# Kernel tuning notes

Hardware: AMD Instinct MI355X
Metric: run time of the kernel (lower is better)

## Reference

```python
import jax, jax.numpy as jnp
import numpy as np

N_NODES = 50000
N_EDGES = 600000
D_FEAT = 128


def setup_inputs() -> dict:
    key = jax.random.key(0)
    k_h, k_src, k_dst, k_dt, k_norm = jax.random.split(key, 5)
    h = jax.random.normal(k_h, (N_NODES, D_FEAT), dtype=jnp.float32)
    src = jax.random.randint(k_src, (N_EDGES,), 0, N_NODES, dtype=jnp.int32)
    dst = jax.random.randint(k_dst, (N_EDGES,), 0, N_NODES, dtype=jnp.int32)
    # dt: non-negative time deltas (scaled up a bit so the decay matters)
    dt = jax.random.uniform(k_dt, (N_EDGES,), dtype=jnp.float32) * 10.0
    # norm: symmetric-normalization-like positive edge weights
    norm = jax.random.uniform(k_norm, (N_EDGES,), dtype=jnp.float32)
    decay_lam = jnp.full((1,), 0.1, dtype=jnp.float32)  # nn.Parameter(0.1)
    return {"h": h, "src": src, "dst": dst, "dt": dt, "norm": norm, "decay_lam": decay_lam}


def reference(h, src, dst, dt, norm, decay_lam):
    # lam = relu(decay_lam) + 1e-4  (scalar)
    lam = jax.nn.relu(decay_lam[0]) + 1e-4
    # per-edge temporal weight: norm * exp(-lam * dt)   [E]
    w = norm * jnp.exp(-lam * dt)
    # u_mul_e: gather source features, scale by edge weight  [E, D]
    m = h[src] * w[:, None]
    # sum-reduce messages at destination nodes  [N, D]
    h_new = jax.ops.segment_sum(m, dst, num_segments=h.shape[0])
    return h_new
```

## Files before the change

### kernel.cpp

```cpp
#include <hip/hip_runtime.h>
#include <hip/hip_bf16.h>

#define D_FEAT 128
#define PAD 32
#define OVF_CAP 4096

typedef float f2v __attribute__((ext_vector_type(2)));

__device__ __forceinline__ unsigned bf16_rne(float f) {
    unsigned u = __float_as_uint(f);
    return (u + 0x7fffu + ((u >> 16) & 1u)) >> 16;
}

__global__ void conv_bucket_kernel(const float* __restrict__ h,
                                   const int* __restrict__ src, const int* __restrict__ dst,
                                   const float* __restrict__ dt, const float* __restrict__ norm,
                                   const float* __restrict__ decay_lam,
                                   unsigned* __restrict__ hb,
                                   int* __restrict__ cursor, unsigned* __restrict__ pairs,
                                   int* __restrict__ ovf_cnt, int* __restrict__ ovf_d,
                                   int* __restrict__ ovf_s, float* __restrict__ ovf_w,
                                   int E, int HN4, int convBlocks) {
    int bid = blockIdx.x;
    if (bid < convBlocks) {
        int i = bid * 256 + threadIdx.x;
        if (i < HN4) {
            float4 v = ((const float4*)h)[i];
            unsigned lo = bf16_rne(v.x) | (bf16_rne(v.y) << 16);
            unsigned hi = bf16_rne(v.z) | (bf16_rne(v.w) << 16);
            ((uint2*)hb)[i] = make_uint2(lo, hi);
        }
    } else {
        int e = (bid - convBlocks) * 256 + threadIdx.x;
        if (e >= E) return;
        float lam = fmaxf(decay_lam[0], 0.0f) + 1e-4f;
        float w = norm[e] * expf(-lam * dt[e]);
        int d = dst[e];
        int s = src[e];
        int pos = atomicAdd(&cursor[d], 1);
        if (pos < PAD) {
            pairs[(size_t)d * PAD + pos] = ((unsigned)s << 16) | bf16_rne(w);
        } else {
            int o = atomicAdd(ovf_cnt, 1);
            if (o < OVF_CAP) { ovf_d[o] = d; ovf_s[o] = s; ovf_w[o] = w; }
        }
    }
}

__global__ void __launch_bounds__(256)
gather_pad_kernel(const unsigned* __restrict__ hb, const int* __restrict__ cursor,
                  const unsigned* __restrict__ pairs,
                  const int* __restrict__ ovf_cnt, const int* __restrict__ ovf_d,
                  const int* __restrict__ ovf_s, const float* __restrict__ ovf_w,
                  float* __restrict__ out, int N) {
    int node = blockIdx.x * 4 + (threadIdx.x >> 6);
    if (node >= N) return;
    int lane = threadIdx.x & 63;
    int deg = cursor[node];
    int m = min(deg, PAD);

    unsigned pu = 0;
    if (lane < m) pu = pairs[(size_t)node * PAD + lane];

    int mr = (m + 7) & ~7;

    float accx = 0.0f, accy = 0.0f;
    for (int j = 0; j < mr; j += 8) {
        unsigned u0 = __shfl(pu, j + 0, 64);
        unsigned u1 = __shfl(pu, j + 1, 64);
        unsigned u2 = __shfl(pu, j + 2, 64);
        unsigned u3 = __shfl(pu, j + 3, 64);
        unsigned u4 = __shfl(pu, j + 4, 64);
        unsigned u5 = __shfl(pu, j + 5, 64);
        unsigned u6 = __shfl(pu, j + 6, 64);
        unsigned u7 = __shfl(pu, j + 7, 64);
        unsigned v0 = hb[(size_t)(u0 >> 16) * 64 + lane];
        unsigned v1 = hb[(size_t)(u1 >> 16) * 64 + lane];
        unsigned v2 = hb[(size_t)(u2 >> 16) * 64 + lane];
        unsigned v3 = hb[(size_t)(u3 >> 16) * 64 + lane];
        unsigned v4 = hb[(size_t)(u4 >> 16) * 64 + lane];
        unsigned v5 = hb[(size_t)(u5 >> 16) * 64 + lane];
        unsigned v6 = hb[(size_t)(u6 >> 16) * 64 + lane];
        unsigned v7 = hb[(size_t)(u7 >> 16) * 64 + lane];
        #define ACC(u, v)                                             \
        {   float wf = __uint_as_float((u) << 16);                    \
            float vx = __uint_as_float((v) << 16);                    \
            float vy = __uint_as_float((v) & 0xffff0000u);            \
            accx += vx * wf; accy += vy * wf; }
        ACC(u0, v0) ACC(u1, v1) ACC(u2, v2) ACC(u3, v3)
        ACC(u4, v4) ACC(u5, v5) ACC(u6, v6) ACC(u7, v7)
        #undef ACC
    }

    if (deg > PAD) {
        int oc = min(*ovf_cnt, OVF_CAP);
        for (int o = 0; o < oc; ++o) {
            if (ovf_d[o] == node) {
                float we = ovf_w[o];
                unsigned v = hb[(size_t)ovf_s[o] * 64 + lane];
                accx += __uint_as_float(v << 16) * we;
                accy += __uint_as_float(v & 0xffff0000u) * we;
            }
        }
    }
    f2v r;
    r.x = accx; r.y = accy;
    __builtin_nontemporal_store(r, (f2v*)(out + (size_t)node * D_FEAT) + lane);
}


__global__ void degree_kernel(const int* __restrict__ dst, int* __restrict__ deg, int E) {
    int e = blockIdx.x * blockDim.x + threadIdx.x;
    if (e >= E) return;
    atomicAdd(&deg[dst[e]], 1);
}

__global__ void scan_blocks(const int* __restrict__ deg, int* __restrict__ offs,
                            int* __restrict__ blockSums, int N) {
    __shared__ int tmp[256];
    int tid = threadIdx.x;
    int gid = blockIdx.x * 256 + tid;
    int v = (gid < N) ? deg[gid] : 0;
    tmp[tid] = v;
    __syncthreads();
    for (int off = 1; off < 256; off <<= 1) {
        int t = (tid >= off) ? tmp[tid - off] : 0;
        __syncthreads();
        tmp[tid] += t;
        __syncthreads();
    }
    if (gid < N) offs[gid] = tmp[tid] - v;
    if (tid == 255) blockSums[blockIdx.x] = tmp[255];
}

__global__ void scan_sums(int* __restrict__ blockSums, int* __restrict__ blockOffs, int nb) {
    __shared__ int tmp[256];
    int tid = threadIdx.x;
    int v = (tid < nb) ? blockSums[tid] : 0;
    tmp[tid] = v;
    __syncthreads();
    for (int off = 1; off < 256; off <<= 1) {
        int t = (tid >= off) ? tmp[tid - off] : 0;
        __syncthreads();
        tmp[tid] += t;
        __syncthreads();
    }
    if (tid < nb) blockOffs[tid] = tmp[tid] - v;
}

__global__ void scan_fixup(int* __restrict__ offs, const int* __restrict__ blockOffs,
                           int* __restrict__ cursor, int N) {
    int gid = blockIdx.x * 256 + threadIdx.x;
    if (gid >= N) return;
    int o = offs[gid] + blockOffs[blockIdx.x];
    offs[gid] = o;
    cursor[gid] = o;
}

__global__ void bucket_kernel(const int* __restrict__ src, const int* __restrict__ dst,
                              const float* __restrict__ dt, const float* __restrict__ norm,
                              const float* __restrict__ decay_lam,
                              int* __restrict__ cursor, float2* __restrict__ pairs, int E) {
    int e = blockIdx.x * blockDim.x + threadIdx.x;
    if (e >= E) return;
    float lam = fmaxf(decay_lam[0], 0.0f) + 1e-4f;
    float w = norm[e] * expf(-lam * dt[e]);
    int d = dst[e];
    int pos = atomicAdd(&cursor[d], 1);
    float2 p;
    p.x = __int_as_float(src[e]);
    p.y = w;
    pairs[pos] = p;
}

__global__ void __launch_bounds__(256)
gather_kernel(const float* __restrict__ h,
              const int* __restrict__ offs, const int* __restrict__ deg,
              const float2* __restrict__ pairs, float* __restrict__ out, int N) {
    int node = blockIdx.x * 4 + (threadIdx.x >> 6);
    if (node >= N) return;
    int lane = threadIdx.x & 63;
    int start = offs[node];
    int end = start + deg[node];
    float accx = 0.0f, accy = 0.0f;
    for (int j = start; j < end; ++j) {
        float2 p = pairs[j];
        int s = __float_as_int(p.x);
        float we = p.y;
        float2 v = ((const float2*)(h + (size_t)s * D_FEAT))[lane];
        accx += v.x * we;
        accy += v.y * we;
    }
    float2 r; r.x = accx; r.y = accy;
    ((float2*)(out + (size_t)node * D_FEAT))[lane] = r;
}

extern "C" void kernel_launch(void* const* d_in, const int* in_sizes, int n_in,
                              void* d_out, int out_size, void* d_ws, size_t ws_size,
                              hipStream_t stream) {
    const float* h         = (const float*)d_in[0];
    const int*   src       = (const int*)d_in[1];
    const int*   dst       = (const int*)d_in[2];
    const float* dt        = (const float*)d_in[3];
    const float* norm      = (const float*)d_in[4];
    const float* decay_lam = (const float*)d_in[5];
    float* out = (float*)d_out;

    const int E  = in_sizes[1];
    const int HN = in_sizes[0];
    const int N  = out_size / D_FEAT;

    size_t pad_need = (size_t)N * 4
                    + 64
                    + (size_t)OVF_CAP * 12
                    + (size_t)N * PAD * 4
                    + (size_t)HN * 2;

    if (ws_size >= pad_need && N <= 65536 && (HN & 3) == 0) {
        char* ws = (char*)d_ws;
        int*      cursor  = (int*)ws;       ws += (size_t)N * 4;
        int*      ovf_cnt = (int*)ws;       ws += 64;
        int*      ovf_d   = (int*)ws;       ws += (size_t)OVF_CAP * 4;
        int*      ovf_s   = (int*)ws;       ws += (size_t)OVF_CAP * 4;
        float*    ovf_w   = (float*)ws;     ws += (size_t)OVF_CAP * 4;
        unsigned* pairs   = (unsigned*)ws;  ws += (size_t)N * PAD * 4;
        unsigned* hb      = (unsigned*)ws;

        hipMemsetAsync(cursor, 0, (size_t)N * 4 + 64, stream);

        const int HN4 = HN / 4;
        const int convBlocks = (HN4 + 255) / 256;
        const int bucketBlocks = (E + 255) / 256;
        conv_bucket_kernel<<<convBlocks + bucketBlocks, 256, 0, stream>>>(
            h, src, dst, dt, norm, decay_lam, hb, cursor, pairs,
            ovf_cnt, ovf_d, ovf_s, ovf_w, E, HN4, convBlocks);

        gather_pad_kernel<<<(N + 3) / 4, 256, 0, stream>>>(
            hb, cursor, pairs, ovf_cnt, ovf_d, ovf_s, ovf_w, out, N);
    } else {
        const int nb = (N + 255) / 256;
        char* ws = (char*)d_ws;
        int*    deg       = (int*)ws;     ws += (size_t)N * 4;
        int*    offs      = (int*)ws;     ws += (size_t)N * 4;
        int*    cursor    = (int*)ws;     ws += (size_t)N * 4;
        int*    blockSums = (int*)ws;     ws += 256 * 4;
        int*    blockOffs = (int*)ws;     ws += 256 * 4;
        float2* pairs     = (float2*)ws;

        hipMemsetAsync(deg, 0, (size_t)N * 4, stream);
        degree_kernel<<<(E + 255) / 256, 256, 0, stream>>>(dst, deg, E);
        scan_blocks<<<nb, 256, 0, stream>>>(deg, offs, blockSums, N);
        scan_sums<<<1, 256, 0, stream>>>(blockSums, blockOffs, nb);
        scan_fixup<<<nb, 256, 0, stream>>>(offs, blockOffs, cursor, N);
        bucket_kernel<<<(E + 255) / 256, 256, 0, stream>>>(
            src, dst, dt, norm, decay_lam, cursor, pairs, E);
        gather_kernel<<<(N + 3) / 4, 256, 0, stream>>>(h, offs, deg, pairs, out, N);
    }
}
```

Before: 156.1 us.

## Replace per-node atomic padded buckets with two-level binned counting sort into CSR

Replaces the per-edge global atomic append into fixed 32-slot per-node buckets with a two-pass sort. Each block first stages 4096 edges in shared memory, bins them by groups of 128 destination nodes, and writes them out with a few global atomics per bin. A per-bin kernel then counting-sorts each bin into a compact CSR with offsets and degrees. The goal is to cut contended global atomics and the scattered padded writes. The cost is an extra kernel launch, extra passes over 8-byte binned entries, and a separate launch for the bf16 conversion of h.

Measured after the change: 130.5 us. 16.4% less time.

```diff
diff --git a/kernel.cpp b/kernel.cpp
--- a/kernel.cpp
+++ b/kernel.cpp
@@ -2,7 +2,11 @@
 #include <hip/hip_bf16.h>
 
 #define D_FEAT 128
-#define PAD 32
+#define BIN_SHIFT 7
+#define NODES_PER_BIN 128
+#define BCAP 4096
+#define EPB 4096
+#define T1 512
 #define OVF_CAP 4096
 
 typedef float f2v __attribute__((ext_vector_type(2)));
@@ -12,56 +16,164 @@
     return (u + 0x7fffu + ((u >> 16) & 1u)) >> 16;
 }
 
-__global__ void conv_bucket_kernel(const float* __restrict__ h,
-                                   const int* __restrict__ src, const int* __restrict__ dst,
-                                   const float* __restrict__ dt, const float* __restrict__ norm,
-                                   const float* __restrict__ decay_lam,
-                                   unsigned* __restrict__ hb,
-                                   int* __restrict__ cursor, unsigned* __restrict__ pairs,
-                                   int* __restrict__ ovf_cnt, int* __restrict__ ovf_d,
-                                   int* __restrict__ ovf_s, float* __restrict__ ovf_w,
-                                   int E, int HN4, int convBlocks) {
-    int bid = blockIdx.x;
-    if (bid < convBlocks) {
-        int i = bid * 256 + threadIdx.x;
-        if (i < HN4) {
-            float4 v = ((const float4*)h)[i];
-            unsigned lo = bf16_rne(v.x) | (bf16_rne(v.y) << 16);
-            unsigned hi = bf16_rne(v.z) | (bf16_rne(v.w) << 16);
-            ((uint2*)hb)[i] = make_uint2(lo, hi);
-        }
-    } else {
-        int e = (bid - convBlocks) * 256 + threadIdx.x;
-        if (e >= E) return;
-        float lam = fmaxf(decay_lam[0], 0.0f) + 1e-4f;
-        float w = norm[e] * expf(-lam * dt[e]);
-        int d = dst[e];
-        int s = src[e];
-        int pos = atomicAdd(&cursor[d], 1);
-        if (pos < PAD) {
-            pairs[(size_t)d * PAD + pos] = ((unsigned)s << 16) | bf16_rne(w);
-        } else {
-            int o = atomicAdd(ovf_cnt, 1);
-            if (o < OVF_CAP) { ovf_d[o] = d; ovf_s[o] = s; ovf_w[o] = w; }
+__global__ void conv_kernel(const float* __restrict__ h, unsigned* __restrict__ hb, int HN4) {
+    int i = blockIdx.x * 256 + threadIdx.x;
+    if (i >= HN4) return;
+    float4 v = ((const float4*)h)[i];
+    ((uint2*)hb)[i] = make_uint2(bf16_rne(v.x) | (bf16_rne(v.y) << 16),
+                                 bf16_rne(v.z) | (bf16_rne(v.w) << 16));
+}
+
+__global__ void __launch_bounds__(T1)
+bin_kernel(const int* __restrict__ src, const int* __restrict__ dst,
+           const float* __restrict__ dt, const float* __restrict__ norm,
+           const float* __restrict__ decay_lam,
+           int* __restrict__ bin_cursor, unsigned long long* __restrict__ binned,
+           int* __restrict__ ovf_cnt, int* __restrict__ ovf_d,
+           int* __restrict__ ovf_s, float* __restrict__ ovf_w,
+           int E, int NB) {
+    __shared__ unsigned hist[T1];
+    __shared__ unsigned tmp[T1];
+    __shared__ unsigned cur[T1];
+    __shared__ unsigned gbase[T1];
+    __shared__ unsigned long long stage[EPB];
+    __shared__ unsigned gaddr[EPB];
+
+    int t = threadIdx.x;
+    int e0 = blockIdx.x * EPB;
+    int cnt_blk = min(EPB, E - e0);
+
+    hist[t] = 0; cur[t] = 0; gbase[t] = 0;
+    __syncthreads();
+
+    float lam = fmaxf(decay_lam[0], 0.0f) + 1e-4f;
+
+    unsigned long long ent[EPB / T1];
+    int bn[EPB / T1];
+    #pragma unroll
+    for (int k = 0; k < EPB / T1; ++k) {
+        int e = e0 + k * T1 + t;
+        bn[k] = -1;
+        if (e < E) {
+            int s = src[e], d = dst[e];
+            float w = norm[e] * expf(-lam * dt[e]);
+            int b = d >> BIN_SHIFT;
+            int l = d & (NODES_PER_BIN - 1);
+            ent[k] = ((unsigned long long)l << 32) | (((unsigned)s << 16) | bf16_rne(w));
+            bn[k] = b;
+            atomicAdd(&hist[b], 1u);
+        }
+    }
+    __syncthreads();
+    tmp[t] = hist[t];
+    __syncthreads();
+    for (int off = 1; off < T1; off <<= 1) {
+        unsigned v = (t >= off) ? tmp[t - off] : 0;
+        __syncthreads();
+        tmp[t] += v;
+        __syncthreads();
+    }
+    unsigned base_t = tmp[t] - hist[t];
+    if (t < NB && hist[t] > 0)
+        gbase[t] = (unsigned)atomicAdd(&bin_cursor[t], (int)hist[t]);
+    __syncthreads();
+    tmp[t] = base_t;
+    __syncthreads();
+
+    #pragma unroll
+    for (int k = 0; k < EPB / T1; ++k) {
+        if (bn[k] >= 0) {
+            int b = bn[k];
+            unsigned loc = atomicAdd(&cur[b], 1u);
+            unsigned p = tmp[b] + loc;
+            unsigned gp = gbase[b] + loc;
+            stage[p] = ent[k];
+            if (gp < BCAP) {
+                gaddr[p] = (unsigned)b * BCAP + gp;
+            } else {
+                gaddr[p] = 0xFFFFFFFFu;
+                int o = atomicAdd(ovf_cnt, 1);
+                if (o < OVF_CAP) {
+                    int l = (int)(ent[k] >> 32);
+                    ovf_d[o] = (b << BIN_SHIFT) | l;
+                    ovf_s[o] = (int)((ent[k] >> 16) & 0xFFFFu);
+                    ovf_w[o] = __uint_as_float(((unsigned)ent[k] & 0xFFFFu) << 16);
+                }
+            }
+        }
+    }
+    __syncthreads();
+    #pragma unroll
+    for (int k = 0; k < EPB / T1; ++k) {
+        int idx = k * T1 + t;
+        if (idx < cnt_blk) {
+            unsigned g = gaddr[idx];
+            if (g != 0xFFFFFFFFu) binned[g] = stage[idx];
         }
     }
 }
 
 __global__ void __launch_bounds__(256)
-gather_pad_kernel(const unsigned* __restrict__ hb, const int* __restrict__ cursor,
-                  const unsigned* __restrict__ pairs,
-                  const int* __restrict__ ovf_cnt, const int* __restrict__ ovf_d,
-                  const int* __restrict__ ovf_s, const float* __restrict__ ovf_w,
-                  float* __restrict__ out, int N) {
+sort_kernel(const unsigned long long* __restrict__ binned, const int* __restrict__ bin_cursor,
+            unsigned* __restrict__ csr, int* __restrict__ offs, int* __restrict__ deg,
+            int N, int NB) {
+    __shared__ unsigned hist[NODES_PER_BIN];
+    __shared__ unsigned tmp[NODES_PER_BIN];
+    __shared__ unsigned cur[NODES_PER_BIN];
+    int b = blockIdx.x;
+    int t = threadIdx.x;
+    int cnt = min(bin_cursor[b], BCAP);
+    if (t < NODES_PER_BIN) { hist[t] = 0; cur[t] = 0; }
+    __syncthreads();
+    size_t base_in = (size_t)b * BCAP;
+    for (int i = t; i < cnt; i += 256) {
+        int l = (int)(binned[base_in + i] >> 32);
+        atomicAdd(&hist[l], 1u);
+    }
+    __syncthreads();
+    if (t < NODES_PER_BIN) tmp[t] = hist[t];
+    __syncthreads();
+    for (int off = 1; off < NODES_PER_BIN; off <<= 1) {
+        unsigned v = 0;
+        if (t < NODES_PER_BIN && t >= off) v = tmp[t - off];
+        __syncthreads();
+        if (t < NODES_PER_BIN) tmp[t] += v;
+        __syncthreads();
+    }
+    if (t < NODES_PER_BIN) {
+        int node = (b << BIN_SHIFT) + t;
+        unsigned loff = tmp[t] - hist[t];
+        if (node < N) {
+            offs[node] = b * BCAP + (int)loff;
+            deg[node]  = (int)hist[t];
+        }
+        tmp[t] = loff;
+    }
+    __syncthreads();
+    for (int i = t; i < cnt; i += 256) {
+        unsigned long long e = binned[base_in + i];
+        int l = (int)(e >> 32);
+        unsigned p = tmp[l] + atomicAdd(&cur[l], 1u);
+        csr[base_in + p] = (unsigned)e;
+    }
+}
+
+__global__ void __launch_bounds__(256)
+gather_kernel2(const unsigned* __restrict__ hb, const int* __restrict__ offs,
+               const int* __restrict__ deg, const unsigned* __restrict__ csr,
+               const int* __restrict__ bin_cursor,
+               const int* __restrict__ ovf_cnt, const int* __restrict__ ovf_d,
+               const int* __restrict__ ovf_s, const float* __restrict__ ovf_w,
+               float* __restrict__ out, int N) {
     int node = blockIdx.x * 4 + (threadIdx.x >> 6);
     if (node >= N) return;
     int lane = threadIdx.x & 63;
-    int deg = cursor[node];
-    int m = min(deg, PAD);
+    int dg = deg[node];
+    int base = offs[node];
+    int m = min(dg, 64);
 
     unsigned pu = 0;
-    if (lane < m) pu = pairs[(size_t)node * PAD + lane];
-
+    if (lane < m) pu = csr[base + lane];
     int mr = (m + 7) & ~7;
 
     float accx = 0.0f, accy = 0.0f;
@@ -91,8 +203,14 @@
         ACC(u4, v4) ACC(u5, v5) ACC(u6, v6) ACC(u7, v7)
         #undef ACC
     }
-
-    if (deg > PAD) {
+    for (int j = 64; j < dg; ++j) {
+        unsigned u = csr[base + j];
+        float wf = __uint_as_float(u << 16);
+        unsigned v = hb[(size_t)(u >> 16) * 64 + lane];
+        accx += __uint_as_float(v << 16) * wf;
+        accy += __uint_as_float(v & 0xffff0000u) * wf;
+    }
+    if (bin_cursor[node >> BIN_SHIFT] > BCAP) {
         int oc = min(*ovf_cnt, OVF_CAP);
         for (int o = 0; o < oc; ++o) {
             if (ovf_d[o] == node) {
@@ -209,51 +327,57 @@
     const int E  = in_sizes[1];
     const int HN = in_sizes[0];
     const int N  = out_size / D_FEAT;
-
-    size_t pad_need = (size_t)N * 4
-                    + 64
-                    + (size_t)OVF_CAP * 12
-                    + (size_t)N * PAD * 4
-                    + (size_t)HN * 2;
-
-    if (ws_size >= pad_need && N <= 65536 && (HN & 3) == 0) {
+    const int NB = (N + NODES_PER_BIN - 1) >> BIN_SHIFT;
+
+    auto align64 = [](size_t x) { return (x + 63) & ~(size_t)63; };
+    size_t sz_binc = align64((size_t)NB * 4);
+    size_t sz_ovfc = 64;
+    size_t sz_ovf  = align64((size_t)OVF_CAP * 4);
+    size_t sz_offs = align64((size_t)N * 4);
+    size_t sz_binn = align64((size_t)NB * BCAP * 8);
+    size_t sz_csr  = align64((size_t)NB * BCAP * 4);
+    size_t sz_hb   = align64((size_t)HN * 2);
+    size_t need = sz_binc + sz_ovfc + 3 * sz_ovf + 2 * sz_offs + sz_binn + sz_csr + sz_hb;
+
+    if (ws_size >= need && N <= 65536 && (HN & 3) == 0) {
         char* ws = (char*)d_ws;
-        int*      cursor  = (int*)ws;       ws += (size_t)N * 4;
-        int*      ovf_cnt = (int*)ws;       ws += 64;
-        int*      ovf_d   = (int*)ws;       ws += (size_t)OVF_CAP * 4;
-        int*      ovf_s   = (int*)ws;       ws += (size_t)OVF_CAP * 4;
-        float*    ovf_w   = (float*)ws;     ws += (size_t)OVF_CAP * 4;
-        unsigned* pairs   = (unsigned*)ws;  ws += (size_t)N * PAD * 4;
-        unsigned* hb      = (unsigned*)ws;
-
-        hipMemsetAsync(cursor, 0, (size_t)N * 4 + 64, stream);
-
-        const int HN4 = HN / 4;
-        const int convBlocks = (HN4 + 255) / 256;
-        const int bucketBlocks = (E + 255) / 256;
-        conv_bucket_kernel<<<convBlocks + bucketBlocks, 256, 0, stream>>>(
-            h, src, dst, dt, norm, decay_lam, hb, cursor, pairs,
-            ovf_cnt, ovf_d, ovf_s, ovf_w, E, HN4, convBlocks);
-
-        gather_pad_kernel<<<(N + 3) / 4, 256, 0, stream>>>(
-            hb, cursor, pairs, ovf_cnt, ovf_d, ovf_s, ovf_w, out, N);
+        int* bin_cursor = (int*)ws;                 ws += sz_binc;
+        int* ovf_cnt    = (int*)ws;                 ws += sz_ovfc;
+        int* ovf_d      = (int*)ws;                 ws += sz_ovf;
+        int* ovf_s      = (int*)ws;                 ws += sz_ovf;
+        float* ovf_w    = (float*)ws;               ws += sz_ovf;
+        int* offs       = (int*)ws;                 ws += sz_offs;
+        int* deg        = (int*)ws;                 ws += sz_offs;
+        unsigned long long* binned = (unsigned long long*)ws;  ws += sz_binn;
+        unsigned* csr   = (unsigned*)ws;            ws += sz_csr;
+        unsigned* hb    = (unsigned*)ws;
+
+        hipMemsetAsync(bin_cursor, 0, sz_binc + sz_ovfc, stream);
+
+        conv_kernel<<<(HN / 4 + 255) / 256, 256, 0, stream>>>(h, hb, HN / 4);
+        bin_kernel<<<(E + EPB - 1) / EPB, T1, 0, stream>>>(
+            src, dst, dt, norm, decay_lam, bin_cursor, binned,
+            ovf_cnt, ovf_d, ovf_s, ovf_w, E, NB);
+        sort_kernel<<<NB, 256, 0, stream>>>(binned, bin_cursor, csr, offs, deg, N, NB);
+        gather_kernel2<<<(N + 3) / 4, 256, 0, stream>>>(
+            hb, offs, deg, csr, bin_cursor, ovf_cnt, ovf_d, ovf_s, ovf_w, out, N);
     } else {
         const int nb = (N + 255) / 256;
         char* ws = (char*)d_ws;
-        int*    deg       = (int*)ws;     ws += (size_t)N * 4;
-        int*    offs      = (int*)ws;     ws += (size_t)N * 4;
+        int*    dega      = (int*)ws;     ws += (size_t)N * 4;
+        int*    offsa     = (int*)ws;     ws += (size_t)N * 4;
         int*    cursor    = (int*)ws;     ws += (size_t)N * 4;
         int*    blockSums = (int*)ws;     ws += 256 * 4;
         int*    blockOffs = (int*)ws;     ws += 256 * 4;
         float2* pairs     = (float2*)ws;
 
-        hipMemsetAsync(deg, 0, (size_t)N * 4, stream);
-        degree_kernel<<<(E + 255) / 256, 256, 0, stream>>>(dst, deg, E);
-        scan_blocks<<<nb, 256, 0, stream>>>(deg, offs, blockSums, N);
+        hipMemsetAsync(dega, 0, (size_t)N * 4, stream);
+        degree_kernel<<<(E + 255) / 256, 256, 0, stream>>>(dst, dega, E);
+        scan_blocks<<<nb, 256, 0, stream>>>(dega, offsa, blockSums, N);
         scan_sums<<<1, 256, 0, stream>>>(blockSums, blockOffs, nb);
-        scan_fixup<<<nb, 256, 0, stream>>>(offs, blockOffs, cursor, N);
+        scan_fixup<<<nb, 256, 0, stream>>>(offsa, blockOffs, cursor, N);
         bucket_kernel<<<(E + 255) / 256, 256, 0, stream>>>(
             src, dst, dt, norm, decay_lam, cursor, pairs, E);
-        gather_kernel<<<(N + 3) / 4, 256, 0, stream>>>(h, offs, deg, pairs, out, N);
-    }
-}
+        gather_kernel<<<(N + 3) / 4, 256, 0, stream>>>(h, offsa, dega, pairs, out, N);
+    }
+}
```
